# Performance work log

Measured on AMD Instinct MI355X. Metric: run time of the kernel, lower is better.

## Reference

```python
import jax, jax.numpy as jnp
import numpy as np

N_NODES = 100000
N_EDGES = 1600000
D = 32


def setup_inputs() -> dict:
    key = jax.random.key(0)
    k1, k2, k3, k4, k5, k6, k7 = jax.random.split(key, 7)
    x = jax.random.normal(k1, (N_NODES, D), dtype=jnp.float32)
    edge_index = jax.random.randint(k2, (2, N_EDGES), 0, N_NODES, dtype=jnp.int64)
    edge_weight = jax.random.uniform(k3, (N_EDGES,), dtype=jnp.float32)
    s = 1.0 / np.sqrt(D)
    W1 = jax.random.uniform(k4, (D, D), jnp.float32, -s, s)
    b1 = jax.random.uniform(k5, (D,), jnp.float32, -s, s)
    W2 = jax.random.uniform(k6, (D, D), jnp.float32, -s, s)
    b2 = jax.random.uniform(k7, (D,), jnp.float32, -s, s)
    return {"x": x, "edge_index": edge_index, "edge_weight": edge_weight,
            "W1": W1, "b1": b1, "W2": W2, "b2": b2}


def reference(x, edge_index, edge_weight, W1, b1, W2, b2):
    N = x.shape[0]
    src, dst = edge_index[0], edge_index[1]
    # gcn_norm with improved=True: self-loops get fill value 2.0
    loops = jnp.arange(N, dtype=edge_index.dtype)
    src_a = jnp.concatenate([src, loops])
    dst_a = jnp.concatenate([dst, loops])
    w_a = jnp.concatenate([edge_weight, jnp.full((N,), 2.0, x.dtype)])
    deg = jax.ops.segment_sum(w_a, dst_a, num_segments=N)          # [N]
    dinv = jnp.where(deg > 0, jax.lax.rsqrt(deg), 0.0)             # deg^-1/2, inf->0
    norm = dinv[src_a] * w_a * dinv[dst_a]                          # [E+N]

    def gcn_conv(h, W, b):
        h = h @ W                                                   # [N,D] dense transform
        msg = h[src_a] * norm[:, None]                              # gather + normalize [E+N,D]
        return jax.ops.segment_sum(msg, dst_a, num_segments=N) + b  # scatter-add + bias

    h = jax.nn.relu(gcn_conv(x, W1, b1))
    h = jax.nn.relu(gcn_conv(h, W2, b2))
    # F.dropout treated as identity (deterministic inference reference)
    return h
```

## Files before the change

### kernel.cpp

```cpp
#include <hip/hip_runtime.h>

#define D       32
#define BS      256
#define CBLK    500
#define CBLKP   500
#define BSH     7
#define BNODES  128
#define MAXBUCK 1024
#define SBUF_CAP 3584
#define ECAP    4096
#define POISON_BASE ((int)0xAAAAAAAAu)

__device__ inline unsigned bf16pack2(float a, float b) {
    unsigned ua = __float_as_uint(a);
    unsigned ub = __float_as_uint(b);
    ua = (ua + 0x7FFFu + ((ua >> 16) & 1)) >> 16;
    ub = (ub + 0x7FFFu + ((ub >> 16) & 1)) >> 16;
    return ua | (ub << 16);
}
__device__ inline uint2 bf16pack4(float4 v) {
    return make_uint2(bf16pack2(v.x, v.y), bf16pack2(v.z, v.w));
}
__device__ inline float4 bf16unpack4(uint2 h) {
    return make_float4(__uint_as_float(h.x << 16),
                       __uint_as_float(h.x & 0xFFFF0000u),
                       __uint_as_float(h.y << 16),
                       __uint_as_float(h.y & 0xFFFF0000u));
}

__device__ inline int lds_excl_scan(int* arr, int L, int* wsum, int t) {
    int carryv = 0;
    for (int base = 0; base < L; base += BS) {
        int idx = base + t;
        int v = (idx < L) ? arr[idx] : 0;
        int incl = v;
#pragma unroll
        for (int off = 1; off < 64; off <<= 1) {
            int u = __shfl_up(incl, off, 64);
            if ((t & 63) >= off) incl += u;
        }
        if ((t & 63) == 63) wsum[t >> 6] = incl;
        __syncthreads();
        int myw = t >> 6;
        int wpre = 0;
        if (myw > 0) wpre += wsum[0];
        if (myw > 1) wpre += wsum[1];
        if (myw > 2) wpre += wsum[2];
        int tot = wsum[0] + wsum[1] + wsum[2] + wsum[3];
        if (idx < L) arr[idx] = carryv + wpre + incl - v;
        __syncthreads();
        carryv += tot;
    }
    return carryv;
}

__global__ void k_localsort_gemm(const int* __restrict__ dst, const int* __restrict__ src,
                                 const float* __restrict__ w, int* __restrict__ bc,
                                 int* __restrict__ locoff, int2* __restrict__ staged,
                                 int E, int EPB, int NBUCK, int NBUCKP,
                                 const float* __restrict__ X, const float* __restrict__ Wm,
                                 uint2* __restrict__ H, int n) {
    __shared__ int    bins[MAXBUCK];
    __shared__ int    wsum[4];
    __shared__ int2   sbuf[SBUF_CAP];
    __shared__ float4 Ws[D * 8];
    int t = threadIdx.x;

    if ((int)blockIdx.x >= CBLK) {
        for (int i = t; i < D * 8; i += BS) Ws[i] = ((const float4*)Wm)[i];
        __syncthreads();
        int gid  = (blockIdx.x - CBLK) * BS + t;
        int node = gid >> 3;
        int q    = gid & 7;
        if (node >= n) return;
        float4 xv  = ((const float4*)X)[node * 8 + q];
        float4 acc = make_float4(0.f, 0.f, 0.f, 0.f);
#pragma unroll
        for (int k = 0; k < D; ++k) {
            float comp = (k & 3) == 0 ? xv.x : (k & 3) == 1 ? xv.y
                       : (k & 3) == 2 ? xv.z : xv.w;
            float  xk = __shfl(comp, k >> 2, 8);
            float4 wr = Ws[k * 8 + q];
            acc.x += xk * wr.x; acc.y += xk * wr.y;
            acc.z += xk * wr.z; acc.w += xk * wr.w;
        }
        H[node * 8 + q] = bf16pack4(acc);
        return;
    }

    int blk = blockIdx.x;
    int beg = blk * EPB;
    int end = min(E, beg + EPB);
    int cnt = end - beg;
    for (int i = t; i < NBUCK; i += BS) bins[i] = 0;
    __syncthreads();

    for (int e = beg + t; e < end; e += BS)
        atomicAdd(&bins[dst[e] >> BSH], 1);
    __syncthreads();
    for (int i = t; i < NBUCK; i += BS) bc[blk * NBUCKP + i] = bins[i];
    __syncthreads();
    lds_excl_scan(bins, NBUCK, wsum, t);
    for (int i = t; i < NBUCK; i += BS) locoff[blk * NBUCKP + i] = bins[i];
    __syncthreads();

    for (int e = beg + t; e < end; e += BS) {
        int dv  = dst[e];
        int b   = dv >> BSH;
        int pos = atomicAdd(&bins[b], 1);
        sbuf[pos] = make_int2(src[e] | ((dv & (BNODES - 1)) << 17), __float_as_int(w[e]));
    }
    __syncthreads();
    int2* myslice = staged + (size_t)blk * EPB;
    for (int i = t; i < cnt; i += BS) myslice[i] = sbuf[i];
}

__global__ void k_trans(const int* __restrict__ bc, const int* __restrict__ locoff,
                        int* __restrict__ bcT, int* __restrict__ locoffT,
                        int* __restrict__ btot, int NBUCK, int NBUCKP) {
    __shared__ int tile[32][33];
    const int* in  = (blockIdx.z == 0) ? bc  : locoff;
    int*       out = (blockIdx.z == 0) ? bcT : locoffT;
    int c0 = blockIdx.x * 32;
    int r0 = blockIdx.y * 32;
    int tx = threadIdx.x & 31, ty = threadIdx.x >> 5;
    for (int dy = ty; dy < 32; dy += 8) {
        int r = r0 + dy, c = c0 + tx;
        tile[dy][tx] = (r < CBLK && c < NBUCK) ? in[r * NBUCKP + c] : 0;
    }
    __syncthreads();
    for (int dy = ty; dy < 32; dy += 8) {
        int c = c0 + dy, r = r0 + tx;
        if (c < NBUCK && r < CBLK) out[c * CBLKP + r] = tile[tx][dy];
    }
    if (blockIdx.z == 0 && ty == 0 && c0 + tx < NBUCK) {
        int s = 0;
#pragma unroll
        for (int dy = 0; dy < 32; ++dy) s += tile[dy][tx];
        if (s) atomicAdd(&btot[c0 + tx], s);
    }
}

__global__ void k_merge(const int* __restrict__ bcT, const int* __restrict__ locoffT,
                        const int* __restrict__ btot, const int2* __restrict__ staged,
                        int2* __restrict__ emeta, int* __restrict__ rowptr,
                        float* __restrict__ dinv, uint2* __restrict__ H,
                        int N, int E, int NBUCK, int EPB) {
    __shared__ int2  ebuf[ECAP];
    __shared__ int   runoff[CBLK];
    __shared__ int   lrun[CBLK];
    __shared__ int   wsum[4];
    __shared__ int   ihist[BNODES];
    __shared__ float fdeg[BNODES];
    __shared__ int   cursor[BNODES];
    __shared__ float sdinv[BNODES];
    __shared__ int   hsum;
    int b = blockIdx.x, t = threadIdx.x;

    for (int k = t; k < CBLK; k += BS) {
        runoff[k] = bcT[b * CBLKP + k];
        lrun[k]   = locoffT[b * CBLKP + k];
    }
    if (t < BNODES) { ihist[t] = 0; fdeg[t] = 0.0f; }

    int pacc = 0;
    for (int k = t; k < b; k += BS) pacc += btot[k];
#pragma unroll
    for (int off = 32; off; off >>= 1) pacc += __shfl_down(pacc, off, 64);
    if ((t & 63) == 0) wsum[t >> 6] = pacc;
    __syncthreads();
    int bstart = wsum[0] + wsum[1] + wsum[2] + wsum[3];
    __syncthreads();

    int total = lds_excl_scan(runoff, CBLK, wsum, t);
    bool fits = total <= ECAP;

    if (fits) {
        for (int p = t; p < total; p += BS) {
            int lo = 0, hi = CBLK - 1;
            while (lo < hi) {
                int mid = (lo + hi + 1) >> 1;
                if (runoff[mid] <= p) lo = mid; else hi = mid - 1;
            }
            int2 v = staged[(size_t)lo * EPB + lrun[lo] + (p - runoff[lo])];
            int local = (v.x >> 17) & (BNODES - 1);
            atomicAdd(&ihist[local], 1);
            atomicAdd(&fdeg[local], __int_as_float(v.y));
            ebuf[p] = v;
        }
    } else {
        for (int k = t; k < CBLK; k += BS) {
            int gs = runoff[k];
            int ge = (k + 1 < CBLK) ? runoff[k + 1] : total;
            const int2* run = staged + (size_t)k * EPB + lrun[k];
            for (int j = 0; j < ge - gs; ++j) {
                int2 v = run[j];
                int local = (v.x >> 17) & (BNODES - 1);
                atomicAdd(&ihist[local], 1);
                atomicAdd(&fdeg[local], __int_as_float(v.y));
            }
        }
    }
    __syncthreads();
    int v128 = 0, incl = 0;
    if (t < BNODES) {
        v128 = ihist[t];
        incl = v128;
#pragma unroll
        for (int off = 1; off < 64; off <<= 1) {
            int u = __shfl_up(incl, off, 64);
            if ((t & 63) >= off) incl += u;
        }
    }
    if (t == 63) hsum = incl;
    __syncthreads();
    if (t < BNODES) {
        if (t >= 64) incl += hsum;
        int excl = incl - v128;
        int node = b * BNODES + t;
        float di = rsqrtf(2.0f + fdeg[t]);
        if (node < N) {
            rowptr[node] = bstart + excl;
            dinv[node]   = di;
        }
        sdinv[t]  = di;
        cursor[t] = excl;
    }
    if (b == NBUCK - 1 && t == 0) rowptr[N] = E;
    __syncthreads();
    {
        int base_node = b * BNODES;
        for (int i = t; i < BNODES * 8; i += BS) {
            int row  = i >> 3;
            int node = base_node + row;
            if (node < N) {
                float di = sdinv[row];
                size_t off = (size_t)node * 8 + (i & 7);
                float4 f = bf16unpack4(H[off]);
                f.x *= di; f.y *= di; f.z *= di; f.w *= di;
                H[off] = bf16pack4(f);
            }
        }
    }
    __syncthreads();
    if (fits) {
        for (int p = t; p < total; p += BS) {
            int2 v = ebuf[p];
            int local = (v.x >> 17) & (BNODES - 1);
            int r = atomicAdd(&cursor[local], 1);
            emeta[bstart + r] = make_int2(v.x & 0x1FFFF, v.y);
        }
    } else {
        for (int k = t; k < CBLK; k += BS) {
            int gs = runoff[k];
            int ge = (k + 1 < CBLK) ? runoff[k + 1] : total;
            const int2* run = staged + (size_t)k * EPB + lrun[k];
            for (int j = 0; j < ge - gs; ++j) {
                int2 v = run[j];
                int local = (v.x >> 17) & (BNODES - 1);
                int r = atomicAdd(&cursor[local], 1);
                emeta[bstart + r] = make_int2(v.x & 0x1FFFF, v.y);
            }
        }
    }
}

template <bool FUSE_GEMM>
__global__ void k_agg(const int* __restrict__ rowptr, const int2* __restrict__ emeta,
                      const uint4* __restrict__ Hs, const float* __restrict__ dinv,
                      const float* __restrict__ b, const float* __restrict__ W2,
                      void* __restrict__ outv, int n) {
    __shared__ float4 Ws[D * 8];
    int tid = threadIdx.x;
    if (FUSE_GEMM) {
        for (int i = tid; i < D * 8; i += BS) Ws[i] = ((const float4*)W2)[i];
        __syncthreads();
    }

    int gid  = blockIdx.x * BS + tid;
    int node = gid >> 2;
    int q    = gid & 3;
    if (node >= n) return;

    float  di  = dinv[node];
    float4 bq0 = ((const float4*)b)[q * 2];
    float4 bq1 = ((const float4*)b)[q * 2 + 1];
    uint4  h0  = Hs[node * 4 + q];
    float4 a0  = bf16unpack4(make_uint2(h0.x, h0.y));
    float4 a1  = bf16unpack4(make_uint2(h0.z, h0.w));
    float4 acc0 = make_float4(2.f * a0.x, 2.f * a0.y, 2.f * a0.z, 2.f * a0.w);
    float4 acc1 = make_float4(2.f * a1.x, 2.f * a1.y, 2.f * a1.z, 2.f * a1.w);

    int beg  = rowptr[node];
    int end  = rowptr[node + 1];
    int full = beg + ((end - beg) & ~7);

    for (int i0 = beg; i0 < full; i0 += 8) {
        int2 em0 = emeta[i0 + q];
        int2 em1 = emeta[i0 + 4 + q];
        float nm0 = __int_as_float(em0.y);
        float nm1 = __int_as_float(em1.y);
#pragma unroll
        for (int j = 0; j < 4; ++j) {
            int   s  = __shfl(em0.x, j, 4);
            float nm = __shfl(nm0, j, 4);
            uint4 hv = Hs[s * 4 + q];
            float4 f0 = bf16unpack4(make_uint2(hv.x, hv.y));
            float4 f1 = bf16unpack4(make_uint2(hv.z, hv.w));
            acc0.x += nm * f0.x; acc0.y += nm * f0.y; acc0.z += nm * f0.z; acc0.w += nm * f0.w;
            acc1.x += nm * f1.x; acc1.y += nm * f1.y; acc1.z += nm * f1.z; acc1.w += nm * f1.w;
        }
#pragma unroll
        for (int j = 0; j < 4; ++j) {
            int   s  = __shfl(em1.x, j, 4);
            float nm = __shfl(nm1, j, 4);
            uint4 hv = Hs[s * 4 + q];
            float4 f0 = bf16unpack4(make_uint2(hv.x, hv.y));
            float4 f1 = bf16unpack4(make_uint2(hv.z, hv.w));
            acc0.x += nm * f0.x; acc0.y += nm * f0.y; acc0.z += nm * f0.z; acc0.w += nm * f0.w;
            acc1.x += nm * f1.x; acc1.y += nm * f1.y; acc1.z += nm * f1.z; acc1.w += nm * f1.w;
        }
    }
    if (full < end) {
        int idx0 = full + q;
        int idx1 = full + 4 + q;
        int2 em0 = (idx0 < end) ? emeta[idx0] : make_int2(0, 0);
        int2 em1 = (idx1 < end) ? emeta[idx1] : make_int2(0, 0);
        float nm0 = (idx0 < end) ? __int_as_float(em0.y) : 0.0f;
        float nm1 = (idx1 < end) ? __int_as_float(em1.y) : 0.0f;
        int rem = end - full;
        int r0 = rem < 4 ? rem : 4;
        for (int j = 0; j < r0; ++j) {
            int   s  = __shfl(em0.x, j, 4);
            float nm = __shfl(nm0, j, 4);
            uint4 hv = Hs[s * 4 + q];
            float4 f0 = bf16unpack4(make_uint2(hv.x, hv.y));
            float4 f1 = bf16unpack4(make_uint2(hv.z, hv.w));
            acc0.x += nm * f0.x; acc0.y += nm * f0.y; acc0.z += nm * f0.z; acc0.w += nm * f0.w;
            acc1.x += nm * f1.x; acc1.y += nm * f1.y; acc1.z += nm * f1.z; acc1.w += nm * f1.w;
        }
        for (int j = 0; j < rem - 4; ++j) {
            int   s  = __shfl(em1.x, j, 4);
            float nm = __shfl(nm1, j, 4);
            uint4 hv = Hs[s * 4 + q];
            float4 f0 = bf16unpack4(make_uint2(hv.x, hv.y));
            float4 f1 = bf16unpack4(make_uint2(hv.z, hv.w));
            acc0.x += nm * f0.x; acc0.y += nm * f0.y; acc0.z += nm * f0.z; acc0.w += nm * f0.w;
            acc1.x += nm * f1.x; acc1.y += nm * f1.y; acc1.z += nm * f1.z; acc1.w += nm * f1.w;
        }
    }
    acc0.x = fmaxf(di * acc0.x + bq0.x, 0.f);
    acc0.y = fmaxf(di * acc0.y + bq0.y, 0.f);
    acc0.z = fmaxf(di * acc0.z + bq0.z, 0.f);
    acc0.w = fmaxf(di * acc0.w + bq0.w, 0.f);
    acc1.x = fmaxf(di * acc1.x + bq1.x, 0.f);
    acc1.y = fmaxf(di * acc1.y + bq1.y, 0.f);
    acc1.z = fmaxf(di * acc1.z + bq1.z, 0.f);
    acc1.w = fmaxf(di * acc1.w + bq1.w, 0.f);

    if (FUSE_GEMM) {
        float4 o0 = make_float4(0.f, 0.f, 0.f, 0.f);
        float4 o1 = make_float4(0.f, 0.f, 0.f, 0.f);
#pragma unroll
        for (int k = 0; k < D; ++k) {
            int sel = k & 7;
            float comp = sel == 0 ? acc0.x : sel == 1 ? acc0.y : sel == 2 ? acc0.z
                       : sel == 3 ? acc0.w : sel == 4 ? acc1.x : sel == 5 ? acc1.y
                       : sel == 6 ? acc1.z : acc1.w;
            float  hk = __shfl(comp, k >> 3, 4);
            float4 w0 = Ws[k * 8 + q * 2];
            float4 w1 = Ws[k * 8 + q * 2 + 1];
            o0.x += hk * w0.x; o0.y += hk * w0.y; o0.z += hk * w0.z; o0.w += hk * w0.w;
            o1.x += hk * w1.x; o1.y += hk * w1.y; o1.z += hk * w1.z; o1.w += hk * w1.w;
        }
        o0.x *= di; o0.y *= di; o0.z *= di; o0.w *= di;
        o1.x *= di; o1.y *= di; o1.z *= di; o1.w *= di;
        ((uint4*)outv)[node * 4 + q] =
            make_uint4(bf16pack2(o0.x, o0.y), bf16pack2(o0.z, o0.w),
                       bf16pack2(o1.x, o1.y), bf16pack2(o1.z, o1.w));
    } else {
        ((float4*)outv)[node * 8 + q * 2]     = acc0;
        ((float4*)outv)[node * 8 + q * 2 + 1] = acc1;
    }
}

__global__ void k_hist_gemm(const int4* __restrict__ dst4, int* __restrict__ cnt,
                            int4* __restrict__ rank4, int E4,
                            const float* __restrict__ X, const float* __restrict__ W,
                            uint2* __restrict__ H, int n, int gE4) {
    __shared__ float4 Ws[D * 8];
    int tid = threadIdx.x;
    if ((int)blockIdx.x < gE4) {
        int i = blockIdx.x * BS + tid;
        if (i >= E4) return;
        int4 d = dst4[i];
        int4 r;
        r.x = atomicAdd(&cnt[d.x], 1) - POISON_BASE;
        r.y = atomicAdd(&cnt[d.y], 1) - POISON_BASE;
        r.z = atomicAdd(&cnt[d.z], 1) - POISON_BASE;
        r.w = atomicAdd(&cnt[d.w], 1) - POISON_BASE;
        rank4[i] = r;
        return;
    }
    for (int i = tid; i < D * 8; i += BS) Ws[i] = ((const float4*)W)[i];
    __syncthreads();
    int gid  = (blockIdx.x - gE4) * BS + tid;
    int node = gid >> 3;
    int q    = gid & 7;
    if (node >= n) return;
    float4 xv  = ((const float4*)X)[node * 8 + q];
    float4 acc = make_float4(0.f, 0.f, 0.f, 0.f);
#pragma unroll
    for (int k = 0; k < D; ++k) {
        float comp = (k & 3) == 0 ? xv.x : (k & 3) == 1 ? xv.y
                   : (k & 3) == 2 ? xv.z : xv.w;
        float  xk = __shfl(comp, k >> 2, 8);
        float4 wr = Ws[k * 8 + q];
        acc.x += xk * wr.x; acc.y += xk * wr.y;
        acc.z += xk * wr.z; acc.w += xk * wr.w;
    }
    H[node * 8 + q] = bf16pack4(acc);
}

__global__ void k_scan1(const int* __restrict__ cnt, int* __restrict__ bsum, int n) {
    __shared__ int s[BS];
    int t = threadIdx.x, i = blockIdx.x * BS + t;
    s[t] = (i < n) ? (cnt[i] - POISON_BASE) : 0;
    __syncthreads();
    for (int off = BS / 2; off > 0; off >>= 1) {
        if (t < off) s[t] += s[t + off];
        __syncthreads();
    }
    if (t == 0) bsum[blockIdx.x] = s[0];
}

__global__ void k_scan23(const int* __restrict__ cnt, const int* __restrict__ bsum,
                         int* __restrict__ rowptr, int n) {
    __shared__ int red[BS];
    __shared__ int s[BS];
    int t = threadIdx.x, i = blockIdx.x * BS + t;
    int pacc = 0;
    for (int k = t; k < (int)blockIdx.x; k += BS) pacc += bsum[k];
    red[t] = pacc;
    __syncthreads();
    for (int off = BS / 2; off > 0; off >>= 1) {
        if (t < off) red[t] += red[t + off];
        __syncthreads();
    }
    int bpre = red[0];
    int v = (i < n) ? (cnt[i] - POISON_BASE) : 0;
    s[t] = v;
    __syncthreads();
    for (int off = 1; off < BS; off <<= 1) {
        int u = (t >= off) ? s[t - off] : 0;
        __syncthreads();
        s[t] += u;
        __syncthreads();
    }
    if (i < n) {
        int excl = bpre + s[t] - v;
        rowptr[i] = excl;
        if (i == n - 1) rowptr[n] = excl + v;
    }
}

__global__ void k_reorder(const int4* __restrict__ src4, const int4* __restrict__ dst4,
                          const float4* __restrict__ w4, const int4* __restrict__ rank4,
                          const int* __restrict__ rowptr, int2* __restrict__ emeta, int E4) {
    int i = blockIdx.x * blockDim.x + threadIdx.x;
    if (i >= E4) return;
    int4   s = src4[i];
    int4   d = dst4[i];
    float4 w = w4[i];
    int4   r = rank4[i];
    emeta[rowptr[d.x] + r.x] = make_int2(s.x, __float_as_int(w.x));
    emeta[rowptr[d.y] + r.y] = make_int2(s.y, __float_as_int(w.y));
    emeta[rowptr[d.z] + r.z] = make_int2(s.z, __float_as_int(w.z));
    emeta[rowptr[d.w] + r.w] = make_int2(s.w, __float_as_int(w.w));
}

__global__ void k_degscaleF(const int* __restrict__ rowptr, const int2* __restrict__ emeta,
                            float* __restrict__ dinv, uint2* __restrict__ H, int n) {
    int gid  = blockIdx.x * blockDim.x + threadIdx.x;
    int node = gid >> 3;
    int c    = gid & 7;
    if (node >= n) return;
    int beg = rowptr[node], end = rowptr[node + 1];
    float sum = 0.0f;
    for (int idx = beg + c; idx < end; idx += 8)
        sum += __int_as_float(emeta[idx].y);
    sum += __shfl_xor(sum, 4, 8);
    sum += __shfl_xor(sum, 2, 8);
    sum += __shfl_xor(sum, 1, 8);
    float di = rsqrtf(2.0f + sum);
    if (c == 0) dinv[node] = di;
    di = __shfl(di, 0, 8);
    size_t off = (size_t)node * 8 + c;
    float4 f = bf16unpack4(H[off]);
    f.x *= di; f.y *= di; f.z *= di; f.w *= di;
    H[off] = bf16pack4(f);
}

extern "C" void kernel_launch(void* const* d_in, const int* in_sizes, int n_in,
                              void* d_out, int out_size, void* d_ws, size_t ws_size,
                              hipStream_t stream) {
    const float* x   = (const float*)d_in[0];
    const int*   ei  = (const int*)d_in[1];
    const float* w   = (const float*)d_in[2];
    const float* W1  = (const float*)d_in[3];
    const float* b1  = (const float*)d_in[4];
    const float* W2  = (const float*)d_in[5];
    const float* b2  = (const float*)d_in[6];
    float*       out = (float*)d_out;

    const int N = in_sizes[0] / D;
    const int E = in_sizes[2];
    const int* src = ei;
    const int* dst = ei + E;

    const int NBUCK  = (N + BNODES - 1) / BNODES;
    const int NBUCKP = (NBUCK + 3) & ~3;
    const int EPB    = (E + CBLK - 1) / CBLK;
    const int NB     = (N + BS - 1) / BS;
    const int E4     = E / 4;
    const int gE4    = (E4 + BS - 1) / BS;
    const int gN8    = (N * 8 + BS - 1) / BS;
    const int gN4    = (N * 4 + BS - 1) / BS;

    char*  base    = (char*)d_ws;
    int2*  emeta   = (int2*)base;
    uint2* ht      = (uint2*)(base + (size_t)E * 8);
    uint2* ht2     = ht + (size_t)N * 8;
    float* dinv    = (float*)(ht2 + (size_t)N * 8);
    int*   rowptr  = (int*)(dinv + N);
    int2*  staged  = (int2*)(rowptr + ((N + 4) & ~3));
    int*   bc      = (int*)(staged + E);
    int*   locoff  = bc + (size_t)CBLK * NBUCKP;
    int*   bcT     = locoff + (size_t)CBLK * NBUCKP;
    int*   locoffT = bcT + (size_t)NBUCK * CBLKP;
    int*   btot    = locoffT + (size_t)NBUCK * CBLKP;
    size_t need    = (size_t)((char*)(btot + NBUCKP) - base);

    bool main_ok = (ws_size >= need) && (NBUCK <= MAXBUCK) && (N < (1 << 17)) &&
                   (EPB <= SBUF_CAP) && (N % 4 == 0);

    if (main_ok) {
        hipMemsetAsync(btot, 0, (size_t)NBUCKP * 4, stream);
        k_localsort_gemm<<<CBLK + gN8, BS, 0, stream>>>(dst, src, w, bc, locoff, staged,
                                                        E, EPB, NBUCK, NBUCKP, x, W1, ht, N);
        dim3 tg((NBUCK + 31) / 32, (CBLK + 31) / 32, 2);
        k_trans<<<tg, BS, 0, stream>>>(bc, locoff, bcT, locoffT, btot, NBUCK, NBUCKP);
        k_merge<<<NBUCK, BS, 0, stream>>>(bcT, locoffT, btot, staged, emeta, rowptr, dinv,
                                          ht, N, E, NBUCK, EPB);
        k_agg<true ><<<gN4, BS, 0, stream>>>(rowptr, emeta, (const uint4*)ht,  dinv, b1, W2, ht2, N);
        k_agg<false><<<gN4, BS, 0, stream>>>(rowptr, emeta, (const uint4*)ht2, dinv, b2, nullptr, out, N);
    } else {
        int* cnt  = (int*)staged;
        int* rank = cnt + N;
        int* bsum = rank + E;
        k_hist_gemm<<<gE4 + gN8, BS, 0, stream>>>((const int4*)dst, cnt, (int4*)rank, E4,
                                                  x, W1, ht, N, gE4);
        k_scan1 <<<NB, BS, 0, stream>>>(cnt, bsum, N);
        k_scan23<<<NB, BS, 0, stream>>>(cnt, bsum, rowptr, N);
        k_reorder<<<(E4 + BS - 1) / BS, BS, 0, stream>>>((const int4*)src, (const int4*)dst,
                                                         (const float4*)w, (const int4*)rank,
                                                         rowptr, emeta, E4);
        k_degscaleF<<<gN8, BS, 0, stream>>>(rowptr, emeta, dinv, ht, N);
        k_agg<true ><<<gN4, BS, 0, stream>>>(rowptr, emeta, (const uint4*)ht,  dinv, b1, W2, ht2, N);
        k_agg<false><<<gN4, BS, 0, stream>>>(rowptr, emeta, (const uint4*)ht2, dinv, b2, nullptr, out, N);
    }
}
```

Measured before the change: 191.4 us.

## Drop transpose kernel, double local-sort blocks, prefetch edge metadata in aggregation

Removes the separate transpose kernel. Bucket totals are now accumulated with global atomics in the local-sort kernel, and the merge kernel reads the per-block count and offset arrays with strided column access. The local-sort grid doubles to 1000 blocks with half the per-block staging buffer, which raises parallelism but also doubles the per-bucket run count each merge block must scan. The aggregation loop also software-prefetches the next group of edge metadata to hide load latency. The strided uncoalesced reads in merge and the larger run count are the main risks.

```diff
diff --git a/kernel.cpp b/kernel.cpp
--- a/kernel.cpp
+++ b/kernel.cpp
@@ -2,12 +2,11 @@
 
 #define D       32
 #define BS      256
-#define CBLK    500
-#define CBLKP   500
+#define CBLK    1000
 #define BSH     7
 #define BNODES  128
 #define MAXBUCK 1024
-#define SBUF_CAP 3584
+#define SBUF_CAP 1792
 #define ECAP    4096
 #define POISON_BASE ((int)0xAAAAAAAAu)
 
@@ -57,6 +56,7 @@
 __global__ void k_localsort_gemm(const int* __restrict__ dst, const int* __restrict__ src,
                                  const float* __restrict__ w, int* __restrict__ bc,
                                  int* __restrict__ locoff, int2* __restrict__ staged,
+                                 int* __restrict__ btot,
                                  int E, int EPB, int NBUCK, int NBUCKP,
                                  const float* __restrict__ X, const float* __restrict__ Wm,
                                  uint2* __restrict__ H, int n) {
@@ -98,7 +98,11 @@
     for (int e = beg + t; e < end; e += BS)
         atomicAdd(&bins[dst[e] >> BSH], 1);
     __syncthreads();
-    for (int i = t; i < NBUCK; i += BS) bc[blk * NBUCKP + i] = bins[i];
+    for (int i = t; i < NBUCK; i += BS) {
+        int v = bins[i];
+        bc[blk * NBUCKP + i] = v;
+        if (v) atomicAdd(&btot[i], v);
+    }
     __syncthreads();
     lds_excl_scan(bins, NBUCK, wsum, t);
     for (int i = t; i < NBUCK; i += BS) locoff[blk * NBUCKP + i] = bins[i];
@@ -115,37 +119,11 @@
     for (int i = t; i < cnt; i += BS) myslice[i] = sbuf[i];
 }
 
-__global__ void k_trans(const int* __restrict__ bc, const int* __restrict__ locoff,
-                        int* __restrict__ bcT, int* __restrict__ locoffT,
-                        int* __restrict__ btot, int NBUCK, int NBUCKP) {
-    __shared__ int tile[32][33];
-    const int* in  = (blockIdx.z == 0) ? bc  : locoff;
-    int*       out = (blockIdx.z == 0) ? bcT : locoffT;
-    int c0 = blockIdx.x * 32;
-    int r0 = blockIdx.y * 32;
-    int tx = threadIdx.x & 31, ty = threadIdx.x >> 5;
-    for (int dy = ty; dy < 32; dy += 8) {
-        int r = r0 + dy, c = c0 + tx;
-        tile[dy][tx] = (r < CBLK && c < NBUCK) ? in[r * NBUCKP + c] : 0;
-    }
-    __syncthreads();
-    for (int dy = ty; dy < 32; dy += 8) {
-        int c = c0 + dy, r = r0 + tx;
-        if (c < NBUCK && r < CBLK) out[c * CBLKP + r] = tile[tx][dy];
-    }
-    if (blockIdx.z == 0 && ty == 0 && c0 + tx < NBUCK) {
-        int s = 0;
-#pragma unroll
-        for (int dy = 0; dy < 32; ++dy) s += tile[dy][tx];
-        if (s) atomicAdd(&btot[c0 + tx], s);
-    }
-}
-
-__global__ void k_merge(const int* __restrict__ bcT, const int* __restrict__ locoffT,
+__global__ void k_merge(const int* __restrict__ bc, const int* __restrict__ locoff,
                         const int* __restrict__ btot, const int2* __restrict__ staged,
                         int2* __restrict__ emeta, int* __restrict__ rowptr,
                         float* __restrict__ dinv, uint2* __restrict__ H,
-                        int N, int E, int NBUCK, int EPB) {
+                        int N, int E, int NBUCK, int NBUCKP, int EPB) {
     __shared__ int2  ebuf[ECAP];
     __shared__ int   runoff[CBLK];
     __shared__ int   lrun[CBLK];
@@ -158,8 +136,8 @@
     int b = blockIdx.x, t = threadIdx.x;
 
     for (int k = t; k < CBLK; k += BS) {
-        runoff[k] = bcT[b * CBLKP + k];
-        lrun[k]   = locoffT[b * CBLKP + k];
+        runoff[k] = bc[(size_t)k * NBUCKP + b];
+        lrun[k]   = locoff[(size_t)k * NBUCKP + b];
     }
     if (t < BNODES) { ihist[t] = 0; fdeg[t] = 0.0f; }
 
@@ -295,14 +273,16 @@
     int end  = rowptr[node + 1];
     int full = beg + ((end - beg) & ~7);
 
+    int2 em0, em1;
+    if (beg < full) { em0 = emeta[beg + q]; em1 = emeta[beg + 4 + q]; }
     for (int i0 = beg; i0 < full; i0 += 8) {
-        int2 em0 = emeta[i0 + q];
-        int2 em1 = emeta[i0 + 4 + q];
-        float nm0 = __int_as_float(em0.y);
-        float nm1 = __int_as_float(em1.y);
+        int2 cem0 = em0, cem1 = em1;
+        if (i0 + 8 < full) { em0 = emeta[i0 + 8 + q]; em1 = emeta[i0 + 12 + q]; }
+        float nm0 = __int_as_float(cem0.y);
+        float nm1 = __int_as_float(cem1.y);
 #pragma unroll
         for (int j = 0; j < 4; ++j) {
-            int   s  = __shfl(em0.x, j, 4);
+            int   s  = __shfl(cem0.x, j, 4);
             float nm = __shfl(nm0, j, 4);
             uint4 hv = Hs[s * 4 + q];
             float4 f0 = bf16unpack4(make_uint2(hv.x, hv.y));
@@ -312,7 +292,7 @@
         }
 #pragma unroll
         for (int j = 0; j < 4; ++j) {
-            int   s  = __shfl(em1.x, j, 4);
+            int   s  = __shfl(cem1.x, j, 4);
             float nm = __shfl(nm1, j, 4);
             uint4 hv = Hs[s * 4 + q];
             float4 f0 = bf16unpack4(make_uint2(hv.x, hv.y));
@@ -324,14 +304,14 @@
     if (full < end) {
         int idx0 = full + q;
         int idx1 = full + 4 + q;
-        int2 em0 = (idx0 < end) ? emeta[idx0] : make_int2(0, 0);
-        int2 em1 = (idx1 < end) ? emeta[idx1] : make_int2(0, 0);
-        float nm0 = (idx0 < end) ? __int_as_float(em0.y) : 0.0f;
-        float nm1 = (idx1 < end) ? __int_as_float(em1.y) : 0.0f;
+        int2 tm0 = (idx0 < end) ? emeta[idx0] : make_int2(0, 0);
+        int2 tm1 = (idx1 < end) ? emeta[idx1] : make_int2(0, 0);
+        float nm0 = (idx0 < end) ? __int_as_float(tm0.y) : 0.0f;
+        float nm1 = (idx1 < end) ? __int_as_float(tm1.y) : 0.0f;
         int rem = end - full;
         int r0 = rem < 4 ? rem : 4;
         for (int j = 0; j < r0; ++j) {
-            int   s  = __shfl(em0.x, j, 4);
+            int   s  = __shfl(tm0.x, j, 4);
             float nm = __shfl(nm0, j, 4);
             uint4 hv = Hs[s * 4 + q];
             float4 f0 = bf16unpack4(make_uint2(hv.x, hv.y));
@@ -340,7 +320,7 @@
             acc1.x += nm * f1.x; acc1.y += nm * f1.y; acc1.z += nm * f1.z; acc1.w += nm * f1.w;
         }
         for (int j = 0; j < rem - 4; ++j) {
-            int   s  = __shfl(em1.x, j, 4);
+            int   s  = __shfl(tm1.x, j, 4);
             float nm = __shfl(nm1, j, 4);
             uint4 hv = Hs[s * 4 + q];
             float4 f0 = bf16unpack4(make_uint2(hv.x, hv.y));
@@ -536,9 +516,7 @@
     int2*  staged  = (int2*)(rowptr + ((N + 4) & ~3));
     int*   bc      = (int*)(staged + E);
     int*   locoff  = bc + (size_t)CBLK * NBUCKP;
-    int*   bcT     = locoff + (size_t)CBLK * NBUCKP;
-    int*   locoffT = bcT + (size_t)NBUCK * CBLKP;
-    int*   btot    = locoffT + (size_t)NBUCK * CBLKP;
+    int*   btot    = locoff + (size_t)CBLK * NBUCKP;
     size_t need    = (size_t)((char*)(btot + NBUCKP) - base);
 
     bool main_ok = (ws_size >= need) && (NBUCK <= MAXBUCK) && (N < (1 << 17)) &&
@@ -547,11 +525,10 @@
     if (main_ok) {
         hipMemsetAsync(btot, 0, (size_t)NBUCKP * 4, stream);
         k_localsort_gemm<<<CBLK + gN8, BS, 0, stream>>>(dst, src, w, bc, locoff, staged,
-                                                        E, EPB, NBUCK, NBUCKP, x, W1, ht, N);
-        dim3 tg((NBUCK + 31) / 32, (CBLK + 31) / 32, 2);
-        k_trans<<<tg, BS, 0, stream>>>(bc, locoff, bcT, locoffT, btot, NBUCK, NBUCKP);
-        k_merge<<<NBUCK, BS, 0, stream>>>(bcT, locoffT, btot, staged, emeta, rowptr, dinv,
-                                          ht, N, E, NBUCK, EPB);
+                                                        btot, E, EPB, NBUCK, NBUCKP,
+                                                        x, W1, ht, N);
+        k_merge<<<NBUCK, BS, 0, stream>>>(bc, locoff, btot, staged, emeta, rowptr, dinv,
+                                          ht, N, E, NBUCK, NBUCKP, EPB);
         k_agg<true ><<<gN4, BS, 0, stream>>>(rowptr, emeta, (const uint4*)ht,  dinv, b1, W2, ht2, N);
         k_agg<false><<<gN4, BS, 0, stream>>>(rowptr, emeta, (const uint4*)ht2, dinv, b2, nullptr, out, N);
     } else {
```

New measurement: 225.2 us. 1.18x slower.
